# Kernel tuning notes

Hardware: AMD Instinct MI355X
Metric: run time of the kernel (lower is better)

Reference implementation:

```python
import jax, jax.numpy as jnp
import numpy as np

B, N, DK, DM = 8, 4096, 512, 64

def setup_inputs() -> dict:
    key = jax.random.key(0)
    ks = jax.random.split(key, 7)
    K = jax.random.normal(ks[0], (B, N, DK), dtype=jnp.float32)
    Q = jax.random.normal(ks[1], (B, N, DK), dtype=jnp.float32)
    V = jax.random.normal(ks[2], (B, N, DK), dtype=jnp.float32)
    s = 1.0 / np.sqrt(DK)
    Wk = jax.random.normal(ks[3], (DM, DK), dtype=jnp.float32) * s
    bk = jax.random.normal(ks[4], (DM,), dtype=jnp.float32) * 0.01
    Wq = jax.random.normal(ks[5], (DM, DK), dtype=jnp.float32) * s
    bq = jax.random.normal(ks[6], (DM,), dtype=jnp.float32) * 0.01
    return {"K": K, "Q": Q, "V": V, "Wk": Wk, "bk": bk, "Wq": Wq, "bq": bq}

def reference(K, Q, V, Wk, bk, Wq, bq):
    # Linear projections (torch Linear: x @ W.T + b)
    pk = jnp.einsum('bnd,md->bnm', K, Wk) + bk  # [B,N,DM]
    pq = jnp.einsum('bnd,md->bnm', Q, Wq) + bq  # [B,M,DM]
    scale = 1.0 / np.sqrt(DM).astype(np.float32)
    scores = jnp.einsum('bqm,bkm->bqk', pq, pk) * scale  # [B,M,N]
    attn = jax.nn.softmax(scores, axis=-1)
    return jnp.einsum('bqk,bkd->bqd', attn, V)  # V unprojected, as in original
```

## Files before the change

kernel.cpp:

```cpp
#include <hip/hip_runtime.h>
#include <hip/hip_bf16.h>
#include <cstdint>


#define DEVINL __device__ __forceinline__

using f32x4  = __attribute__((ext_vector_type(4)))  float;
using bf16x8 = __attribute__((ext_vector_type(8)))  short;
using bf16x4 = __attribute__((ext_vector_type(4)))  short;

constexpr int BATCH = 8;
constexpr int N     = 4096;
constexpr int DK    = 512;
constexpr int DM    = 64;
constexpr int KVB   = 64;
constexpr int QB    = 128;
constexpr int STEPS = N / KVB;

DEVINL short cvt_bf16(float x) {
  uint32_t u = __float_as_uint(x);
  uint32_t r = u + 0x7fffu + ((u >> 16) & 1u);
  return (short)(r >> 16);
}

DEVINL void async16(void* lds, const void* g) {
  __builtin_amdgcn_global_load_lds(
      (const __attribute__((address_space(1))) uint32_t*)(uintptr_t)g,
      (__attribute__((address_space(3))) uint32_t*)(uint32_t)(uintptr_t)lds,
      16, 0, 0);
}

DEVINL f32x4 mfma16(bf16x8 a, bf16x8 b, f32x4 c) {
  return __builtin_amdgcn_mfma_f32_16x16x32_bf16(a, b, c, 0, 0, 0);
}

__global__ __launch_bounds__(256) void wconv_kernel(
    const float* __restrict__ Wk, const float* __restrict__ Wq,
    short* __restrict__ WkB, short* __restrict__ WqB) {
  int i = blockIdx.x * 256 + threadIdx.x;
  WkB[i] = cvt_bf16(Wk[i]);
  WqB[i] = cvt_bf16(Wq[i]);
}

__global__ __launch_bounds__(256) void vtrans_kernel(
    const float* __restrict__ V, short* __restrict__ Vt) {
  int bb = blockIdx.x;
  int b  = bb >> 9;
  int nt = (bb >> 3) & 63;
  int dt = bb & 7;
  int n0 = nt * 64, d0 = dt * 64;
  __shared__ short t_lds[64][80];
  int tid = threadIdx.x;
#pragma unroll
  for (int it = 0; it < 4; ++it) {
    int idx = it * 256 + tid;
    int row = idx >> 4;
    int c4  = idx & 15;
    f32x4 v = *(const f32x4*)&V[((size_t)b * N + n0 + row) * DK + d0 + c4 * 4];
#pragma unroll
    for (int j = 0; j < 4; ++j) t_lds[c4 * 4 + j][row] = cvt_bf16(v[j]);
  }
  __syncthreads();
#pragma unroll
  for (int it = 0; it < 2; ++it) {
    int idx = it * 256 + tid;
    int rd = idx >> 3;
    int ck = idx & 7;
    bf16x8 vv = *(const bf16x8*)&t_lds[rd][ck * 8];
    *(bf16x8*)&Vt[((size_t)b * DK + d0 + rd) * N + n0 + ck * 8] = vv;
  }
}

__global__ __launch_bounds__(512, 2) void proj_kernel(
    const float* __restrict__ Q, const float* __restrict__ K,
    const short* __restrict__ WqB, const short* __restrict__ WkB,
    const float* __restrict__ bq, const float* __restrict__ bk,
    short* __restrict__ pq, short* __restrict__ pk) {
  bool isK = blockIdx.x >= 256;
  const float* X    = isK ? K : Q;
  const short* W    = isK ? WkB : WqB;
  const float* bias = isK ? bk : bq;
  short* P          = isK ? pk : pq;
  float sc          = isK ? 1.0f : 0.125f;
  int rb = (blockIdx.x & 255) * 128;

  __shared__ short x_lds[128 * 512];
  int tid = threadIdx.x, w = tid >> 6, lane = tid & 63, g = lane >> 4, c = lane & 15;

#pragma unroll
  for (int it = 0; it < 32; ++it) {
    int idx4 = it * 512 + tid;
    int row  = idx4 >> 7;
    int col  = (idx4 & 127) * 4;
    f32x4 v = *(const f32x4*)&X[((size_t)rb + row) * DK + col];
    bf16x4 hb;
#pragma unroll
    for (int j = 0; j < 4; ++j) hb[j] = cvt_bf16(v[j]);
    int scz = (col >> 3) ^ (row & 7);
    *(bf16x4*)&x_lds[row * 512 + scz * 8 + ((col >> 2) & 1) * 4] = hb;
  }
  __syncthreads();

  f32x4 o[4];
#pragma unroll
  for (int mt = 0; mt < 4; ++mt) o[mt] = f32x4{0.f, 0.f, 0.f, 0.f};
  int arow = w * 16 + c;
#pragma unroll
  for (int ks = 0; ks < 16; ++ks) {
    int scz = (ks * 4 + g) ^ (arow & 7);
    bf16x8 a = *(const bf16x8*)&x_lds[arow * 512 + scz * 8];
#pragma unroll
    for (int mt = 0; mt < 4; ++mt) {
      bf16x8 bfr = *(const bf16x8*)&W[(size_t)(mt * 16 + c) * DK + ks * 32 + g * 8];
      o[mt] = mfma16(a, bfr, o[mt]);
    }
  }
#pragma unroll
  for (int mt = 0; mt < 4; ++mt) {
    float bb = bias[mt * 16 + c];
#pragma unroll
    for (int r = 0; r < 4; ++r) {
      int row = rb + w * 16 + g * 4 + r;
      P[(size_t)row * DM + mt * 16 + c] = cvt_bf16((o[mt][r] + bb) * sc);
    }
  }
}

__global__ __launch_bounds__(512, 2) void flash_kernel(
    const short* __restrict__ pq, const short* __restrict__ pk,
    const short* __restrict__ vt, float* __restrict__ out) {
  int b  = blockIdx.x & 7;
  int qt = blockIdx.x >> 3;
  int q0 = qt * QB;

  int tid = threadIdx.x, w = tid >> 6, lane = tid & 63, g = lane >> 4, c = lane & 15;
  int qrow = w * 16 + c;

  __shared__ short pk_lds[KVB * DM];
  __shared__ short vt_lds[2][DK * KVB];
  __shared__ short p_lds[QB * KVB];
  __shared__ float alpha_lds[QB];
  __shared__ float lsum_lds[QB];

  const short* pk_b = pk + (size_t)b * N * DM;
  const short* vt_b = vt + (size_t)b * DK * N;

  const short* pq_row = pq + ((size_t)b * N + q0 + qrow) * DM;
  bf16x8 qf0 = *(const bf16x8*)(pq_row + g * 8);
  bf16x8 qf1 = *(const bf16x8*)(pq_row + 32 + g * 8);

  f32x4 acc[4][8];
#pragma unroll
  for (int i = 0; i < 4; ++i)
#pragma unroll
    for (int j = 0; j < 8; ++j) acc[i][j] = f32x4{0.f, 0.f, 0.f, 0.f};

  float m_run = -1e30f, l_run = 0.f;

  auto stage_pk = [&](int t) {
    int row = tid >> 3, ck = tid & 7;
    const short* src = pk_b + (size_t)(t * KVB + row) * DM + ((ck ^ (row & 7)) * 8);
    async16((void*)(pk_lds + (size_t)w * 512), (const void*)src);
  };
  auto stage_vt = [&](int t, int buf) {
#pragma unroll
    for (int r = 0; r < 8; ++r) {
      int off16 = r * 512 + tid;
      int row = off16 >> 3, ck = off16 & 7;
      const short* src = vt_b + (size_t)row * N + t * KVB + ((ck ^ (row & 7)) * 8);
      async16((void*)(&vt_lds[buf][0] + (size_t)(r * 512 + w * 64) * 8), (const void*)src);
    }
  };

  stage_pk(0);
  stage_vt(0, 0);
  __syncthreads();

  float sv[16];
  bf16x4 pb[4];
  float alpha;
  {
#pragma unroll
    for (int s = 0; s < 4; ++s) {
      int row = s * 16 + c;
      bf16x8 a0 = *(const bf16x8*)&pk_lds[row * 64 + ((g ^ (row & 7)) * 8)];
      bf16x8 a1 = *(const bf16x8*)&pk_lds[row * 64 + (((4 + g) ^ (row & 7)) * 8)];
      f32x4 d = f32x4{0.f, 0.f, 0.f, 0.f};
      d = mfma16(a0, qf0, d);
      d = mfma16(a1, qf1, d);
#pragma unroll
      for (int r = 0; r < 4; ++r) sv[s * 4 + r] = d[r];
    }
    float tmax = sv[0];
#pragma unroll
    for (int j = 1; j < 16; ++j) tmax = fmaxf(tmax, sv[j]);
    tmax = fmaxf(tmax, __shfl_xor(tmax, 16));
    tmax = fmaxf(tmax, __shfl_xor(tmax, 32));
    m_run = tmax;
    float ts = 0.f;
#pragma unroll
    for (int j = 0; j < 16; ++j) { sv[j] = __expf(sv[j] - m_run); ts += sv[j]; }
    ts += __shfl_xor(ts, 16);
    ts += __shfl_xor(ts, 32);
    l_run = ts;
    alpha = 1.0f;
#pragma unroll
    for (int s = 0; s < 4; ++s)
#pragma unroll
      for (int r = 0; r < 4; ++r) pb[s][r] = cvt_bf16(sv[s * 4 + r]);
  }
  asm volatile("s_waitcnt lgkmcnt(0)" ::: "memory");
  __builtin_amdgcn_s_barrier();
#pragma unroll
  for (int s = 0; s < 4; ++s) {
    int ck = (s * 2 + (g >> 1)) ^ (qrow & 7);
    *(bf16x4*)&p_lds[qrow * 64 + ck * 8 + (g & 1) * 4] = pb[s];
  }
  if (g == 0) alpha_lds[qrow] = alpha;
  stage_pk(1);
  asm volatile("s_waitcnt lgkmcnt(0)" ::: "memory");
  __builtin_amdgcn_s_barrier();
  __builtin_amdgcn_sched_barrier(0);

  for (int t = 0; t < STEPS - 1; ++t) {
    int vb = t & 1;
    stage_vt(t + 1, vb ^ 1);
    asm volatile("s_waitcnt vmcnt(8)" ::: "memory");
    __builtin_amdgcn_sched_barrier(0);

    {
      float al[8];
      bool ne = false;
#pragma unroll
      for (int j = 0; j < 8; ++j) { al[j] = alpha_lds[j * 16 + c]; ne |= (al[j] != 1.0f); }
      if (__any(ne)) {
#pragma unroll
        for (int i = 0; i < 4; ++i)
#pragma unroll
          for (int j = 0; j < 8; ++j) acc[i][j] *= al[j];
      }
    }

#pragma unroll
    for (int s = 0; s < 4; ++s) {
      int row = s * 16 + c;
      bf16x8 a0 = *(const bf16x8*)&pk_lds[row * 64 + ((g ^ (row & 7)) * 8)];
      bf16x8 a1 = *(const bf16x8*)&pk_lds[row * 64 + (((4 + g) ^ (row & 7)) * 8)];
      f32x4 d = f32x4{0.f, 0.f, 0.f, 0.f};
      d = mfma16(a0, qf0, d);
      d = mfma16(a1, qf1, d);
#pragma unroll
      for (int r = 0; r < 4; ++r) sv[s * 4 + r] = d[r];
    }

    float tmax = sv[0];
#pragma unroll
    for (int j = 1; j < 16; ++j) tmax = fmaxf(tmax, sv[j]);
    tmax = fmaxf(tmax, __shfl_xor(tmax, 16));
    tmax = fmaxf(tmax, __shfl_xor(tmax, 32));
    alpha = 1.0f;
    if (tmax > m_run + 8.0f) {
      alpha = __expf(m_run - tmax);
      m_run = tmax;
    }

    __builtin_amdgcn_s_setprio(1);
    {
      bf16x8 pf[8];
#pragma unroll
      for (int j = 0; j < 8; ++j) {
        int row = j * 16 + c;
        pf[j] = *(const bf16x8*)&p_lds[row * 64 + ((g ^ (row & 7)) * 8)];
      }
#pragma unroll
      for (int i = 0; i < 4; ++i) {
        int row = w * 64 + i * 16 + c;
        bf16x8 vf = *(const bf16x8*)&vt_lds[vb][row * 64 + ((g ^ (row & 7)) * 8)];
#pragma unroll
        for (int j = 0; j < 8; ++j) acc[i][j] = mfma16(vf, pf[j], acc[i][j]);
      }
    }
    __builtin_amdgcn_s_setprio(0);

    float ts = 0.f;
#pragma unroll
    for (int j = 0; j < 16; ++j) { sv[j] = __expf(sv[j] - m_run); ts += sv[j]; }

    __builtin_amdgcn_s_setprio(1);
    {
      bf16x8 pf[8];
#pragma unroll
      for (int j = 0; j < 8; ++j) {
        int row = j * 16 + c;
        pf[j] = *(const bf16x8*)&p_lds[row * 64 + (((4 + g) ^ (row & 7)) * 8)];
      }
#pragma unroll
      for (int i = 0; i < 4; ++i) {
        int row = w * 64 + i * 16 + c;
        bf16x8 vf = *(const bf16x8*)&vt_lds[vb][row * 64 + (((4 + g) ^ (row & 7)) * 8)];
#pragma unroll
        for (int j = 0; j < 8; ++j) acc[i][j] = mfma16(vf, pf[j], acc[i][j]);
      }
    }
    __builtin_amdgcn_s_setprio(0);

    ts += __shfl_xor(ts, 16);
    ts += __shfl_xor(ts, 32);
    l_run = l_run * alpha + ts;
#pragma unroll
    for (int s = 0; s < 4; ++s)
#pragma unroll
      for (int r = 0; r < 4; ++r) pb[s][r] = cvt_bf16(sv[s * 4 + r]);

    asm volatile("s_waitcnt lgkmcnt(0)" ::: "memory");
    __builtin_amdgcn_s_barrier();
    __builtin_amdgcn_sched_barrier(0);

#pragma unroll
    for (int s = 0; s < 4; ++s) {
      int ck = (s * 2 + (g >> 1)) ^ (qrow & 7);
      *(bf16x4*)&p_lds[qrow * 64 + ck * 8 + (g & 1) * 4] = pb[s];
    }
    if (g == 0) alpha_lds[qrow] = alpha;
    if (t < STEPS - 2) stage_pk(t + 2);
    asm volatile("s_waitcnt lgkmcnt(0)" ::: "memory");
    __builtin_amdgcn_s_barrier();
    __builtin_amdgcn_sched_barrier(0);
  }

  asm volatile("s_waitcnt vmcnt(0)" ::: "memory");
  __builtin_amdgcn_sched_barrier(0);
  {
    float al[8];
    bool ne = false;
#pragma unroll
    for (int j = 0; j < 8; ++j) { al[j] = alpha_lds[j * 16 + c]; ne |= (al[j] != 1.0f); }
    if (__any(ne)) {
#pragma unroll
      for (int i = 0; i < 4; ++i)
#pragma unroll
        for (int j = 0; j < 8; ++j) acc[i][j] *= al[j];
    }
  }
  {
    int vb = (STEPS - 1) & 1;
#pragma unroll
    for (int kh = 0; kh < 2; ++kh) {
      bf16x8 pf[8];
#pragma unroll
      for (int j = 0; j < 8; ++j) {
        int row = j * 16 + c;
        pf[j] = *(const bf16x8*)&p_lds[row * 64 + (((kh * 4 + g) ^ (row & 7)) * 8)];
      }
#pragma unroll
      for (int i = 0; i < 4; ++i) {
        int row = w * 64 + i * 16 + c;
        bf16x8 vf = *(const bf16x8*)&vt_lds[vb][row * 64 + (((kh * 4 + g) ^ (row & 7)) * 8)];
#pragma unroll
        for (int j = 0; j < 8; ++j) acc[i][j] = mfma16(vf, pf[j], acc[i][j]);
      }
    }
  }

  if (g == 0) lsum_lds[qrow] = l_run;
  asm volatile("s_waitcnt lgkmcnt(0)" ::: "memory");
  __builtin_amdgcn_s_barrier();

  float* out_b = out + (size_t)b * N * DK;
#pragma unroll
  for (int j = 0; j < 8; ++j) {
    float rl = 1.f / lsum_lds[j * 16 + c];
#pragma unroll
    for (int i = 0; i < 4; ++i)
#pragma unroll
      for (int r = 0; r < 4; ++r) {
        int q    = q0 + j * 16 + c;
        int vcol = w * 64 + i * 16 + g * 4 + r;
        out_b[(size_t)q * DK + vcol] = acc[i][j][r] * rl;
      }
  }
}

extern "C" void kernel_launch(void* const* d_in, const int* in_sizes, int n_in,
                              void* d_out, int out_size, void* d_ws, size_t ws_size,
                              hipStream_t stream) {
  (void)in_sizes; (void)n_in; (void)out_size; (void)ws_size;
  const float* K  = (const float*)d_in[0];
  const float* Q  = (const float*)d_in[1];
  const float* V  = (const float*)d_in[2];
  const float* Wk = (const float*)d_in[3];
  const float* bk = (const float*)d_in[4];
  const float* Wq = (const float*)d_in[5];
  const float* bq = (const float*)d_in[6];
  float* out = (float*)d_out;

  char* ws = (char*)d_ws;
  short* pq  = (short*)(ws + 0);
  short* pk  = (short*)(ws + ((size_t)4 << 20));
  short* vt  = (short*)(ws + ((size_t)8 << 20));
  short* WqB = (short*)(ws + ((size_t)40 << 20));
  short* WkB = (short*)(ws + ((size_t)40 << 20) + 64 * 512 * 2);

  hipLaunchKernelGGL(wconv_kernel,  dim3(128),  dim3(256), 0, stream, Wk, Wq, WkB, WqB);
  hipLaunchKernelGGL(vtrans_kernel, dim3(4096), dim3(256), 0, stream, V, vt);
  hipLaunchKernelGGL(proj_kernel,   dim3(512),  dim3(512), 0, stream, Q, K, WqB, WkB, bq, bk, pq, pk);
  hipLaunchKernelGGL(flash_kernel,  dim3(256),  dim3(512), 0, stream, pq, pk, vt, out);
}
```

Baseline: 248.7 us.

## Fold log2e into Q scale, use exp2, packed bf16 converts, precomputed LDS addresses

Folds log2(e) into the Q projection scale so softmax can use exp2f instead of __expf, and raises the deferred-rescale threshold to match. Replaces per-element bf16 rounding with the packed v_cvt_pk_bf16_f32 instruction. Precomputes swizzled LDS and global addresses outside the loop and replaces per-lane alpha reads with a per-wave flag byte. Also vectorizes the output stores to 16-byte writes and raises priority around the QK MFMAs. These cut VALU and address arithmetic in the inner loop, at the cost of more live registers.

```diff
diff --git a/kernel.cpp b/kernel.cpp
--- a/kernel.cpp
+++ b/kernel.cpp
@@ -17,10 +17,19 @@
 constexpr int QB    = 128;
 constexpr int STEPS = N / KVB;
 
+#define PQ_SCALE 0.18033688011112042f
+#define DEFER_THR 11.5f
+
 DEVINL short cvt_bf16(float x) {
   uint32_t u = __float_as_uint(x);
   uint32_t r = u + 0x7fffu + ((u >> 16) & 1u);
   return (short)(r >> 16);
+}
+
+DEVINL uint32_t cvtpk(float lo, float hi) {
+  uint32_t r;
+  asm("v_cvt_pk_bf16_f32 %0, %1, %2" : "=v"(r) : "v"(lo), "v"(hi));
+  return r;
 }
 
 DEVINL void async16(void* lds, const void* g) {
@@ -81,7 +90,7 @@
   const short* W    = isK ? WkB : WqB;
   const float* bias = isK ? bk : bq;
   short* P          = isK ? pk : pq;
-  float sc          = isK ? 1.0f : 0.125f;
+  float sc          = isK ? 1.0f : PQ_SCALE;
   int rb = (blockIdx.x & 255) * 128;
 
   __shared__ short x_lds[128 * 512];
@@ -135,15 +144,50 @@
 
   int tid = threadIdx.x, w = tid >> 6, lane = tid & 63, g = lane >> 4, c = lane & 15;
   int qrow = w * 16 + c;
+  int cs = c & 7;
 
   __shared__ short pk_lds[KVB * DM];
   __shared__ short vt_lds[2][DK * KVB];
   __shared__ short p_lds[QB * KVB];
   __shared__ float alpha_lds[QB];
   __shared__ float lsum_lds[QB];
-
-  const short* pk_b = pk + (size_t)b * N * DM;
-  const short* vt_b = vt + (size_t)b * DK * N;
+  __shared__ unsigned long long aflag8;
+
+  const short* pkr0 = pk_lds + c * 64 + ((g ^ cs) * 8);
+  const short* pkr1 = pk_lds + c * 64 + (((4 + g) ^ cs) * 8);
+  const short* pfr0 = p_lds + c * 64 + ((g ^ cs) * 8);
+  const short* pfr1 = p_lds + c * 64 + (((4 + g) ^ cs) * 8);
+  const short* vfA0 = &vt_lds[0][(w * 64 + c) * 64 + ((g ^ cs) * 8)];
+  const short* vfA1 = &vt_lds[0][(w * 64 + c) * 64 + (((4 + g) ^ cs) * 8)];
+  const short* vfB0 = vfA0 + DK * KVB;
+  const short* vfB1 = vfA1 + DK * KVB;
+  short* pw0 = p_lds + qrow * 64 + ((((g >> 1) + 0) ^ cs) * 8) + (g & 1) * 4;
+  short* pw1 = p_lds + qrow * 64 + ((((g >> 1) + 2) ^ cs) * 8) + (g & 1) * 4;
+  short* pw2 = p_lds + qrow * 64 + ((((g >> 1) + 4) ^ cs) * 8) + (g & 1) * 4;
+  short* pw3 = p_lds + qrow * 64 + ((((g >> 1) + 6) ^ cs) * 8) + (g & 1) * 4;
+
+  const short* pk_base = pk + (size_t)b * N * DM;
+  const short* vt_base = vt + (size_t)b * DK * N;
+  int tr = tid >> 3, tc = tid & 7;
+  int pk_vo = tr * 64 + ((tc ^ (tr & 7)) * 8);
+  int vt_vo[8];
+#pragma unroll
+  for (int r = 0; r < 8; ++r)
+    vt_vo[r] = (r * 64 + tr) * N + ((tc ^ (tr & 7)) * 8);
+  short* pk_dst = pk_lds + w * 512;
+  short* vt_dst0 = &vt_lds[0][w * 512];
+  short* vt_dst1 = &vt_lds[1][w * 512];
+
+  auto stage_pk = [&]() {
+    async16((void*)pk_dst, (const void*)(pk_base + pk_vo));
+    pk_base += KVB * DM;
+  };
+  auto stage_vt = [&](short* vdst) {
+#pragma unroll
+    for (int r = 0; r < 8; ++r)
+      async16((void*)(vdst + r * 4096), (const void*)(vt_base + vt_vo[r]));
+    vt_base += KVB;
+  };
 
   const short* pq_row = pq + ((size_t)b * N + q0 + qrow) * DM;
   bf16x8 qf0 = *(const bf16x8*)(pq_row + g * 8);
@@ -156,35 +200,19 @@
     for (int j = 0; j < 8; ++j) acc[i][j] = f32x4{0.f, 0.f, 0.f, 0.f};
 
   float m_run = -1e30f, l_run = 0.f;
-
-  auto stage_pk = [&](int t) {
-    int row = tid >> 3, ck = tid & 7;
-    const short* src = pk_b + (size_t)(t * KVB + row) * DM + ((ck ^ (row & 7)) * 8);
-    async16((void*)(pk_lds + (size_t)w * 512), (const void*)src);
-  };
-  auto stage_vt = [&](int t, int buf) {
-#pragma unroll
-    for (int r = 0; r < 8; ++r) {
-      int off16 = r * 512 + tid;
-      int row = off16 >> 3, ck = off16 & 7;
-      const short* src = vt_b + (size_t)row * N + t * KVB + ((ck ^ (row & 7)) * 8);
-      async16((void*)(&vt_lds[buf][0] + (size_t)(r * 512 + w * 64) * 8), (const void*)src);
-    }
-  };
-
-  stage_pk(0);
-  stage_vt(0, 0);
+  float sv[16];
+  uint32_t pbu[8];
+  float alpha;
+
+  stage_pk();
+  stage_vt(vt_dst0);
   __syncthreads();
 
-  float sv[16];
-  bf16x4 pb[4];
-  float alpha;
   {
 #pragma unroll
     for (int s = 0; s < 4; ++s) {
-      int row = s * 16 + c;
-      bf16x8 a0 = *(const bf16x8*)&pk_lds[row * 64 + ((g ^ (row & 7)) * 8)];
-      bf16x8 a1 = *(const bf16x8*)&pk_lds[row * 64 + (((4 + g) ^ (row & 7)) * 8)];
+      bf16x8 a0 = *(const bf16x8*)(pkr0 + s * 1024);
+      bf16x8 a1 = *(const bf16x8*)(pkr1 + s * 1024);
       f32x4 d = f32x4{0.f, 0.f, 0.f, 0.f};
       d = mfma16(a0, qf0, d);
       d = mfma16(a1, qf1, d);
@@ -199,41 +227,42 @@
     m_run = tmax;
     float ts = 0.f;
 #pragma unroll
-    for (int j = 0; j < 16; ++j) { sv[j] = __expf(sv[j] - m_run); ts += sv[j]; }
+    for (int j = 0; j < 16; ++j) { sv[j] = exp2f(sv[j] - m_run); ts += sv[j]; }
     ts += __shfl_xor(ts, 16);
     ts += __shfl_xor(ts, 32);
     l_run = ts;
     alpha = 1.0f;
 #pragma unroll
-    for (int s = 0; s < 4; ++s)
-#pragma unroll
-      for (int r = 0; r < 4; ++r) pb[s][r] = cvt_bf16(sv[s * 4 + r]);
+    for (int s = 0; s < 4; ++s) {
+      pbu[s * 2]     = cvtpk(sv[s * 4 + 0], sv[s * 4 + 1]);
+      pbu[s * 2 + 1] = cvtpk(sv[s * 4 + 2], sv[s * 4 + 3]);
+    }
   }
   asm volatile("s_waitcnt lgkmcnt(0)" ::: "memory");
   __builtin_amdgcn_s_barrier();
-#pragma unroll
-  for (int s = 0; s < 4; ++s) {
-    int ck = (s * 2 + (g >> 1)) ^ (qrow & 7);
-    *(bf16x4*)&p_lds[qrow * 64 + ck * 8 + (g & 1) * 4] = pb[s];
-  }
-  if (g == 0) alpha_lds[qrow] = alpha;
-  stage_pk(1);
+  *(uint32_t*)pw0 = pbu[0]; *(uint32_t*)(pw0 + 2) = pbu[1];
+  *(uint32_t*)pw1 = pbu[2]; *(uint32_t*)(pw1 + 2) = pbu[3];
+  *(uint32_t*)pw2 = pbu[4]; *(uint32_t*)(pw2 + 2) = pbu[5];
+  *(uint32_t*)pw3 = pbu[6]; *(uint32_t*)(pw3 + 2) = pbu[7];
+  if (lane == 0) ((unsigned char*)&aflag8)[w] = 0;
+  if (g == 0) alpha_lds[qrow] = 1.0f;
+  stage_pk();
   asm volatile("s_waitcnt lgkmcnt(0)" ::: "memory");
   __builtin_amdgcn_s_barrier();
   __builtin_amdgcn_sched_barrier(0);
 
   for (int t = 0; t < STEPS - 1; ++t) {
     int vb = t & 1;
-    stage_vt(t + 1, vb ^ 1);
+    stage_vt(vb ? vt_dst0 : vt_dst1);
     asm volatile("s_waitcnt vmcnt(8)" ::: "memory");
     __builtin_amdgcn_sched_barrier(0);
 
     {
-      float al[8];
-      bool ne = false;
-#pragma unroll
-      for (int j = 0; j < 8; ++j) { al[j] = alpha_lds[j * 16 + c]; ne |= (al[j] != 1.0f); }
-      if (__any(ne)) {
+      unsigned long long f = aflag8;
+      if (f) {
+        float al[8];
+#pragma unroll
+        for (int j = 0; j < 8; ++j) al[j] = alpha_lds[j * 16 + c];
 #pragma unroll
         for (int i = 0; i < 4; ++i)
 #pragma unroll
@@ -241,65 +270,61 @@
       }
     }
 
+    __builtin_amdgcn_s_setprio(1);
 #pragma unroll
     for (int s = 0; s < 4; ++s) {
-      int row = s * 16 + c;
-      bf16x8 a0 = *(const bf16x8*)&pk_lds[row * 64 + ((g ^ (row & 7)) * 8)];
-      bf16x8 a1 = *(const bf16x8*)&pk_lds[row * 64 + (((4 + g) ^ (row & 7)) * 8)];
+      bf16x8 a0 = *(const bf16x8*)(pkr0 + s * 1024);
+      bf16x8 a1 = *(const bf16x8*)(pkr1 + s * 1024);
       f32x4 d = f32x4{0.f, 0.f, 0.f, 0.f};
       d = mfma16(a0, qf0, d);
       d = mfma16(a1, qf1, d);
 #pragma unroll
       for (int r = 0; r < 4; ++r) sv[s * 4 + r] = d[r];
     }
-
-    float tmax = sv[0];
-#pragma unroll
-    for (int j = 1; j < 16; ++j) tmax = fmaxf(tmax, sv[j]);
+    __builtin_amdgcn_s_setprio(0);
+
+    float tmax = fmaxf(fmaxf(fmaxf(sv[0], sv[1]), fmaxf(sv[2], sv[3])),
+                       fmaxf(fmaxf(sv[4], sv[5]), fmaxf(sv[6], sv[7])));
+    tmax = fmaxf(tmax, fmaxf(fmaxf(fmaxf(sv[8], sv[9]), fmaxf(sv[10], sv[11])),
+                             fmaxf(fmaxf(sv[12], sv[13]), fmaxf(sv[14], sv[15]))));
     tmax = fmaxf(tmax, __shfl_xor(tmax, 16));
     tmax = fmaxf(tmax, __shfl_xor(tmax, 32));
     alpha = 1.0f;
-    if (tmax > m_run + 8.0f) {
-      alpha = __expf(m_run - tmax);
+    if (tmax > m_run + DEFER_THR) {
+      alpha = exp2f(m_run - tmax);
       m_run = tmax;
     }
 
+    const short* vf0 = vb ? vfB0 : vfA0;
+    const short* vf1 = vb ? vfB1 : vfA1;
     __builtin_amdgcn_s_setprio(1);
     {
       bf16x8 pf[8];
 #pragma unroll
-      for (int j = 0; j < 8; ++j) {
-        int row = j * 16 + c;
-        pf[j] = *(const bf16x8*)&p_lds[row * 64 + ((g ^ (row & 7)) * 8)];
+      for (int j = 0; j < 8; ++j) pf[j] = *(const bf16x8*)(pfr0 + j * 1024);
+#pragma unroll
+      for (int i = 0; i < 4; ++i) {
+        bf16x8 vfr = *(const bf16x8*)(vf0 + i * 1024);
+#pragma unroll
+        for (int j = 0; j < 8; ++j) acc[i][j] = mfma16(vfr, pf[j], acc[i][j]);
       }
+    }
+    __builtin_amdgcn_s_setprio(0);
+
+    float ts = 0.f;
+#pragma unroll
+    for (int j = 0; j < 16; ++j) { sv[j] = exp2f(sv[j] - m_run); ts += sv[j]; }
+
+    __builtin_amdgcn_s_setprio(1);
+    {
+      bf16x8 pf[8];
+#pragma unroll
+      for (int j = 0; j < 8; ++j) pf[j] = *(const bf16x8*)(pfr1 + j * 1024);
 #pragma unroll
       for (int i = 0; i < 4; ++i) {
-        int row = w * 64 + i * 16 + c;
-        bf16x8 vf = *(const bf16x8*)&vt_lds[vb][row * 64 + ((g ^ (row & 7)) * 8)];
-#pragma unroll
-        for (int j = 0; j < 8; ++j) acc[i][j] = mfma16(vf, pf[j], acc[i][j]);
-      }
-    }
-    __builtin_amdgcn_s_setprio(0);
-
-    float ts = 0.f;
-#pragma unroll
-    for (int j = 0; j < 16; ++j) { sv[j] = __expf(sv[j] - m_run); ts += sv[j]; }
-
-    __builtin_amdgcn_s_setprio(1);
-    {
-      bf16x8 pf[8];
-#pragma unroll
-      for (int j = 0; j < 8; ++j) {
-        int row = j * 16 + c;
-        pf[j] = *(const bf16x8*)&p_lds[row * 64 + (((4 + g) ^ (row & 7)) * 8)];
-      }
-#pragma unroll
-      for (int i = 0; i < 4; ++i) {
-        int row = w * 64 + i * 16 + c;
-        bf16x8 vf = *(const bf16x8*)&vt_lds[vb][row * 64 + (((4 + g) ^ (row & 7)) * 8)];
-#pragma unroll
-        for (int j = 0; j < 8; ++j) acc[i][j] = mfma16(vf, pf[j], acc[i][j]);
+        bf16x8 vfr = *(const bf16x8*)(vf1 + i * 1024);
+#pragma unroll
+        for (int j = 0; j < 8; ++j) acc[i][j] = mfma16(vfr, pf[j], acc[i][j]);
       }
     }
     __builtin_amdgcn_s_setprio(0);
@@ -308,21 +333,25 @@
     ts += __shfl_xor(ts, 32);
     l_run = l_run * alpha + ts;
 #pragma unroll
-    for (int s = 0; s < 4; ++s)
-#pragma unroll
-      for (int r = 0; r < 4; ++r) pb[s][r] = cvt_bf16(sv[s * 4 + r]);
+    for (int s = 0; s < 4; ++s) {
+      pbu[s * 2]     = cvtpk(sv[s * 4 + 0], sv[s * 4 + 1]);
+      pbu[s * 2 + 1] = cvtpk(sv[s * 4 + 2], sv[s * 4 + 3]);
+    }
 
     asm volatile("s_waitcnt lgkmcnt(0)" ::: "memory");
     __builtin_amdgcn_s_barrier();
     __builtin_amdgcn_sched_barrier(0);
 
-#pragma unroll
-    for (int s = 0; s < 4; ++s) {
-      int ck = (s * 2 + (g >> 1)) ^ (qrow & 7);
-      *(bf16x4*)&p_lds[qrow * 64 + ck * 8 + (g & 1) * 4] = pb[s];
-    }
+    *(uint32_t*)pw0 = pbu[0]; *(uint32_t*)(pw0 + 2) = pbu[1];
+    *(uint32_t*)pw1 = pbu[2]; *(uint32_t*)(pw1 + 2) = pbu[3];
+    *(uint32_t*)pw2 = pbu[4]; *(uint32_t*)(pw2 + 2) = pbu[5];
+    *(uint32_t*)pw3 = pbu[6]; *(uint32_t*)(pw3 + 2) = pbu[7];
     if (g == 0) alpha_lds[qrow] = alpha;
-    if (t < STEPS - 2) stage_pk(t + 2);
+    {
+      int any = __any(alpha != 1.0f);
+      if (lane == 0) ((unsigned char*)&aflag8)[w] = (unsigned char)any;
+    }
+    if (t < STEPS - 2) stage_pk();
     asm volatile("s_waitcnt lgkmcnt(0)" ::: "memory");
     __builtin_amdgcn_s_barrier();
     __builtin_amdgcn_sched_barrier(0);
@@ -331,11 +360,11 @@
   asm volatile("s_waitcnt vmcnt(0)" ::: "memory");
   __builtin_amdgcn_sched_barrier(0);
   {
-    float al[8];
-    bool ne = false;
-#pragma unroll
-    for (int j = 0; j < 8; ++j) { al[j] = alpha_lds[j * 16 + c]; ne |= (al[j] != 1.0f); }
-    if (__any(ne)) {
+    unsigned long long f = aflag8;
+    if (f) {
+      float al[8];
+#pragma unroll
+      for (int j = 0; j < 8; ++j) al[j] = alpha_lds[j * 16 + c];
 #pragma unroll
       for (int i = 0; i < 4; ++i)
 #pragma unroll
@@ -344,20 +373,28 @@
   }
   {
     int vb = (STEPS - 1) & 1;
-#pragma unroll
-    for (int kh = 0; kh < 2; ++kh) {
+    const short* vf0 = vb ? vfB0 : vfA0;
+    const short* vf1 = vb ? vfB1 : vfA1;
+    {
       bf16x8 pf[8];
 #pragma unroll
-      for (int j = 0; j < 8; ++j) {
-        int row = j * 16 + c;
-        pf[j] = *(const bf16x8*)&p_lds[row * 64 + (((kh * 4 + g) ^ (row & 7)) * 8)];
+      for (int j = 0; j < 8; ++j) pf[j] = *(const bf16x8*)(pfr0 + j * 1024);
+#pragma unroll
+      for (int i = 0; i < 4; ++i) {
+        bf16x8 vfr = *(const bf16x8*)(vf0 + i * 1024);
+#pragma unroll
+        for (int j = 0; j < 8; ++j) acc[i][j] = mfma16(vfr, pf[j], acc[i][j]);
       }
+    }
+    {
+      bf16x8 pf[8];
+#pragma unroll
+      for (int j = 0; j < 8; ++j) pf[j] = *(const bf16x8*)(pfr1 + j * 1024);
 #pragma unroll
       for (int i = 0; i < 4; ++i) {
-        int row = w * 64 + i * 16 + c;
-        bf16x8 vf = *(const bf16x8*)&vt_lds[vb][row * 64 + (((kh * 4 + g) ^ (row & 7)) * 8)];
-#pragma unroll
-        for (int j = 0; j < 8; ++j) acc[i][j] = mfma16(vf, pf[j], acc[i][j]);
+        bf16x8 vfr = *(const bf16x8*)(vf1 + i * 1024);
+#pragma unroll
+        for (int j = 0; j < 8; ++j) acc[i][j] = mfma16(vfr, pf[j], acc[i][j]);
       }
     }
   }
@@ -370,14 +407,13 @@
 #pragma unroll
   for (int j = 0; j < 8; ++j) {
     float rl = 1.f / lsum_lds[j * 16 + c];
-#pragma unroll
-    for (int i = 0; i < 4; ++i)
-#pragma unroll
-      for (int r = 0; r < 4; ++r) {
-        int q    = q0 + j * 16 + c;
-        int vcol = w * 64 + i * 16 + g * 4 + r;
-        out_b[(size_t)q * DK + vcol] = acc[i][j][r] * rl;
-      }
+    int q = q0 + j * 16 + c;
+#pragma unroll
+    for (int i = 0; i < 4; ++i) {
+      f32x4 o = acc[i][j];
+      o[0] *= rl; o[1] *= rl; o[2] *= rl; o[3] *= rl;
+      *(f32x4*)&out_b[(size_t)q * DK + w * 64 + i * 16 + g * 4] = o;
+    }
   }
 }
 
```

Result: slower. 254.0 us (+2.1%).
